# Kernel tuning notes

Hardware: AMD Instinct MI355X
Metric: run time of the kernel (lower is better)

The kernel has to match this reference:

```python
import jax, jax.numpy as jnp
import numpy as np

DIM = 512
HEADS = 8
DH = DIM // HEADS          # 64
M = DIM // 2               # 256 landmarks
PINV_ITERS = 6
KERNEL = 33                # residual_conv_kernel (lucidrains default)
SCALE = DH ** -0.5
LN_EPS = 1e-5


def setup_inputs() -> dict:
    key = jax.random.key(0)
    ks = jax.random.split(key, 6)
    b, n = 4, 4096
    x = jax.random.normal(ks[0], (b, n, DIM), jnp.float32)
    ln_w = jnp.ones((DIM,), jnp.float32)
    ln_b = jnp.zeros((DIM,), jnp.float32)
    w_qkv = jax.random.normal(ks[1], (DIM, 3 * DIM), jnp.float32) / np.float32(np.sqrt(DIM))
    w_out = jax.random.normal(ks[2], (DIM, DIM), jnp.float32) / np.float32(np.sqrt(DIM))
    b_out = jnp.zeros((DIM,), jnp.float32)
    # depthwise Conv2d(heads, heads, (33,1), groups=heads, bias=False): OIHW = (8,1,33,1)
    conv_w = jax.random.normal(ks[3], (HEADS, 1, KERNEL, 1), jnp.float32) / np.float32(np.sqrt(KERNEL))
    # admin_torch.as_module(8): residual x*omega + f(x), omega learnable scalar init sqrt(8)
    omega = jnp.asarray(np.sqrt(8.0), jnp.float32)
    return dict(x=x, ln_w=ln_w, ln_b=ln_b, w_qkv=w_qkv, w_out=w_out,
                b_out=b_out, conv_w=conv_w, omega=omega)


def _layernorm(x, w, b):
    mu = x.mean(-1, keepdims=True)
    var = x.var(-1, keepdims=True)
    return (x - mu) * jax.lax.rsqrt(var + LN_EPS) * w + b


def _moore_penrose_pinv(x, iters):
    # Newton-Schulz iteration, exactly as lucidrains nystrom-attention
    abs_x = jnp.abs(x)
    col = abs_x.sum(-1)
    row = abs_x.sum(-2)
    z = jnp.swapaxes(x, -1, -2) / (jnp.max(col) * jnp.max(row))
    I = jnp.eye(x.shape[-1], dtype=x.dtype)
    for _ in range(iters):
        xz = x @ z
        z = 0.25 * z @ (13. * I - xz @ (15. * I - xz @ (7. * I - xz)))
    return z


def reference(x, ln_w, ln_b, w_qkv, w_out, b_out, conv_w, omega):
    b, n, _ = x.shape
    nx = _layernorm(x, ln_w, ln_b)
    qkv = nx @ w_qkv                                # [b, n, 3*dim]
    q, k, v = jnp.split(qkv, 3, axis=-1)
    to_heads = lambda t: t.reshape(b, n, HEADS, DH).transpose(0, 2, 1, 3)  # bhnd
    q = to_heads(q) * SCALE
    k = to_heads(k)
    v = to_heads(v)
    l = n // M                                      # tokens per landmark group
    q_l = q.reshape(b, HEADS, M, l, DH).mean(3)     # [b,h,m,d]
    k_l = k.reshape(b, HEADS, M, l, DH).mean(3)
    sim1 = jnp.einsum('bhid,bhjd->bhij', q, k_l)    # [b,h,n,m]
    sim2 = jnp.einsum('bhid,bhjd->bhij', q_l, k_l)  # [b,h,m,m]
    sim3 = jnp.einsum('bhid,bhjd->bhij', q_l, k)    # [b,h,m,n]
    a1 = jax.nn.softmax(sim1, -1)
    a2 = jax.nn.softmax(sim2, -1)
    a3 = jax.nn.softmax(sim3, -1)
    a2_inv = _moore_penrose_pinv(a2, PINV_ITERS)
    out = (a1 @ a2_inv) @ (a3 @ v)                  # [b,h,n,d]
    # residual depthwise conv along the sequence dim of v
    res = jax.lax.conv_general_dilated(
        v, conv_w, window_strides=(1, 1),
        padding=((KERNEL // 2, KERNEL // 2), (0, 0)),
        dimension_numbers=('NCHW', 'OIHW', 'NCHW'),
        feature_group_count=HEADS)
    out = out + res
    out = out.transpose(0, 2, 1, 3).reshape(b, n, HEADS * DH)
    out = out @ w_out + b_out                       # to_out (dropout is eval no-op)
    return x * omega + out                          # admin residual
```

## Files before the change

kernel.cpp:

```cpp
#include <hip/hip_runtime.h>
#include <math.h>

#define B_    4
#define N_    4096
#define DIM_  512
#define H_    8
#define DH_   64
#define M_    256
#define LGRP  16
#define BH_   (B_*H_)
#define SCALE_ 0.125f
#define LN_EPS_ 1e-5f

#define SZ_QKVH (B_*H_*N_*DH_)
#define SZ_LM   (BH_*M_*DH_)
#define SZ_MM   (BH_*M_*M_)

typedef unsigned short ushort_t;
typedef __attribute__((ext_vector_type(8))) short bfrag8;
typedef __attribute__((ext_vector_type(4))) float fvec4;

__device__ __forceinline__ ushort_t f2b(float f) {
    unsigned u = __float_as_uint(f);
    unsigned r = (u + 0x7fffu + ((u >> 16) & 1u)) >> 16;
    return (ushort_t)r;
}
__device__ __forceinline__ float b2f(ushort_t s) {
    return __uint_as_float(((unsigned)s) << 16);
}

__global__ __launch_bounds__(256) void ln_kernel(const float* __restrict__ x,
                                                 const float* __restrict__ w,
                                                 const float* __restrict__ bb,
                                                 ushort_t* __restrict__ nxb) {
    int row = blockIdx.x;
    int t = threadIdx.x;
    const float* xr = x + (size_t)row * DIM_;
    float v0 = xr[t], v1 = xr[t + 256];
    float s = v0 + v1, sq = v0 * v0 + v1 * v1;
    __shared__ float ls[4], lq[4];
    for (int off = 32; off > 0; off >>= 1) {
        s  += __shfl_down(s, off);
        sq += __shfl_down(sq, off);
    }
    int wid = t >> 6, lid = t & 63;
    if (lid == 0) { ls[wid] = s; lq[wid] = sq; }
    __syncthreads();
    if (t == 0) {
        float S = 0, Q = 0;
        for (int i = 0; i < 4; i++) { S += ls[i]; Q += lq[i]; }
        ls[0] = S; lq[0] = Q;
    }
    __syncthreads();
    float mean = ls[0] * (1.f / DIM_);
    float var  = lq[0] * (1.f / DIM_) - mean * mean;
    float rs = rsqrtf(var + LN_EPS_);
    ushort_t* o = nxb + (size_t)row * DIM_;
    o[t]       = f2b((v0 - mean) * rs * w[t]       + bb[t]);
    o[t + 256] = f2b((v1 - mean) * rs * w[t + 256] + bb[t + 256]);
}

__global__ __launch_bounds__(256) void tcast(const float* __restrict__ in,
                                             ushort_t* __restrict__ outT,
                                             int R, int C) {
    __shared__ float tile[32][33];
    int c0 = blockIdx.x * 32, r0 = blockIdx.y * 32;
    int t = threadIdx.x;
    #pragma unroll
    for (int u = 0; u < 4; u++) {
        int lin = t + 256 * u;
        int r = lin >> 5, c = lin & 31;
        tile[r][c] = in[(size_t)(r0 + r) * C + c0 + c];
    }
    __syncthreads();
    #pragma unroll
    for (int u = 0; u < 4; u++) {
        int lin = t + 256 * u;
        int cc = lin >> 5, rr = lin & 31;
        outT[(size_t)(c0 + cc) * R + r0 + rr] = f2b(tile[rr][cc]);
    }
}

template<int EPI>
__global__ __launch_bounds__(256) void gemm_bt128(const ushort_t* __restrict__ A,
                                                  const ushort_t* __restrict__ BT,
                                                  ushort_t* __restrict__ qb,
                                                  ushort_t* __restrict__ kb,
                                                  ushort_t* __restrict__ vb,
                                                  const float* __restrict__ x,
                                                  const float* __restrict__ bo,
                                                  const float* __restrict__ omega,
                                                  float* __restrict__ out) {
    const int K = 512;
    __shared__ __align__(16) ushort_t smem[2 * 128 * 72];
    ushort_t (*As)[72] = (ushort_t(*)[72])smem;
    ushort_t (*Bs)[72] = (ushort_t(*)[72])(smem + 128 * 72);
    int t = threadIdx.x;
    int n0 = blockIdx.x * 128, m0 = blockIdx.y * 128;
    int w = t >> 6, lane = t & 63;
    int wr = (w >> 1) * 64, wc = (w & 1) * 64;
    int l15 = lane & 15, quad = lane >> 4, kq = quad * 8;
    fvec4 acc[4][4] = {};
    int rbase = t >> 3, c8 = (t & 7) * 8;

    for (int kc = 0; kc < K; kc += 64) {
        #pragma unroll
        for (int u = 0; u < 4; u++) {
            int rr = rbase + 32 * u;
            const ushort_t* ga;
            if (EPI == 0) {
                ga = A + (size_t)(m0 + rr) * K + kc + c8;
            } else {
                int grow = m0 + rr; int b_ = grow >> 12, nn = grow & 4095;
                int col = kc + c8; int hd = col >> 6, dd = col & 63;
                ga = A + (((size_t)(b_ * H_ + hd) * N_ + nn) << 6) + dd;
            }
            *(float4*)&As[rr][c8] = *(const float4*)ga;
            *(float4*)&Bs[rr][c8] = *(const float4*)(BT + (size_t)(n0 + rr) * K + kc + c8);
        }
        __syncthreads();
        #pragma unroll
        for (int ks = 0; ks < 64; ks += 32) {
            bfrag8 a[4], b[4];
            #pragma unroll
            for (int r = 0; r < 4; r++) a[r] = *(bfrag8*)&As[wr + r * 16 + l15][ks + kq];
            #pragma unroll
            for (int c = 0; c < 4; c++) b[c] = *(bfrag8*)&Bs[wc + c * 16 + l15][ks + kq];
            #pragma unroll
            for (int r = 0; r < 4; r++)
                #pragma unroll
                for (int c = 0; c < 4; c++)
                    acc[r][c] = __builtin_amdgcn_mfma_f32_16x16x32_bf16(a[r], b[c], acc[r][c], 0, 0, 0);
        }
        __syncthreads();
    }

    if (EPI == 0) {
        int sec = n0 >> 9;
        float mul = (sec == 0) ? SCALE_ : 1.0f;
        ushort_t (*Ct)[132] = (ushort_t(*)[132])smem;
        #pragma unroll
        for (int r = 0; r < 4; r++) {
            #pragma unroll
            for (int reg = 0; reg < 4; reg++) {
                int lr = wr + r * 16 + quad * 4 + reg;
                #pragma unroll
                for (int c = 0; c < 4; c++) {
                    int lc = wc + c * 16 + l15;
                    Ct[lr][lc] = f2b(acc[r][c][reg] * mul);
                }
            }
        }
        __syncthreads();
        int row = t & 127, half = t >> 7;
        int grow = m0 + row; int b_ = grow >> 12, nn = grow & 4095;
        int head = ((n0 & 511) >> 6) + half;
        ushort_t* dstbuf = (sec == 0) ? qb : ((sec == 1) ? kb : vb);
        ushort_t* dp = dstbuf + (((size_t)(b_ * H_ + head) * N_ + nn) << 6);
        #pragma unroll
        for (int i = 0; i < 8; i++)
            *(uint4*)(dp + i * 8) = *(uint4*)&Ct[row][half * 64 + i * 8];
    } else {
        float om = omega[0];
        #pragma unroll
        for (int r = 0; r < 4; r++) {
            #pragma unroll
            for (int reg = 0; reg < 4; reg++) {
                int grow = m0 + wr + r * 16 + quad * 4 + reg;
                #pragma unroll
                for (int c = 0; c < 4; c++) {
                    int gcol = n0 + wc + c * 16 + l15;
                    size_t o = (size_t)grow * DIM_ + gcol;
                    out[o] = om * x[o] + bo[gcol] + acc[r][c][reg];
                }
            }
        }
    }
}

__global__ __launch_bounds__(256) void landmark_kernel(const ushort_t* __restrict__ q,
                                                       const ushort_t* __restrict__ k,
                                                       ushort_t* __restrict__ ql,
                                                       ushort_t* __restrict__ kl) {
    int idx = blockIdx.x * 256 + threadIdx.x;
    const ushort_t* src = blockIdx.y ? k : q;
    ushort_t* dst = blockIdx.y ? kl : ql;
    int d8 = (idx & 7) * 8;
    int m = (idx >> 3) & 255;
    int bh = idx >> 11;
    const ushort_t* p = src + (((size_t)bh * N_) + m * LGRP) * DH_ + d8;
    float s[8] = {};
    #pragma unroll
    for (int j = 0; j < LGRP; j++) {
        union { uint4 u4; ushort_t sv[8]; } val;
        val.u4 = *(const uint4*)(p + (size_t)j * DH_);
        #pragma unroll
        for (int e = 0; e < 8; e++) s[e] += b2f(val.sv[e]);
    }
    union { uint4 u4; ushort_t sv[8]; } o;
    #pragma unroll
    for (int e = 0; e < 8; e++) o.sv[e] = f2b(s[e] * (1.f / LGRP));
    *(uint4*)(dst + ((size_t)bh * M_ + m) * DH_ + d8) = o.u4;
}

__global__ __launch_bounds__(256) void sim2_softmax(const ushort_t* __restrict__ ql,
                                                    const ushort_t* __restrict__ kl,
                                                    float* __restrict__ a2,
                                                    ushort_t* __restrict__ a2b) {
    int i = blockIdx.x, bh = blockIdx.y, j = threadIdx.x;
    __shared__ float qrow[64];
    __shared__ float red[256];
    if (j < 64) qrow[j] = b2f(ql[((size_t)bh * M_ + i) * DH_ + j]);
    __syncthreads();
    const ushort_t* kr = kl + ((size_t)bh * M_ + j) * DH_;
    float s = 0;
    #pragma unroll
    for (int d = 0; d < 64; d++) s += qrow[d] * b2f(kr[d]);
    red[j] = s; __syncthreads();
    for (int off = 128; off > 0; off >>= 1) {
        if (j < off) red[j] = fmaxf(red[j], red[j + off]);
        __syncthreads();
    }
    float mx = red[0]; __syncthreads();
    float p = __expf(s - mx);
    red[j] = p; __syncthreads();
    for (int off = 128; off > 0; off >>= 1) {
        if (j < off) red[j] += red[j + off];
        __syncthreads();
    }
    float res = p / red[0];
    size_t o = ((size_t)bh * M_ + i) * M_ + j;
    a2[o] = res;
    a2b[o] = f2b(res);
}

__global__ void zero2(unsigned* p) { if (threadIdx.x < 2) p[threadIdx.x] = 0u; }

__global__ __launch_bounds__(256) void a2_maxes(const float* __restrict__ a2, unsigned* red) {
    int bh = blockIdx.x, t = threadIdx.x;
    const float* A = a2 + (size_t)bh * M_ * M_;
    float rs = 0, cs = 0;
    for (int j = 0; j < M_; j++) rs += A[t * M_ + j];
    for (int i = 0; i < M_; i++) cs += A[i * M_ + t];
    __shared__ float lr[256], lc[256];
    lr[t] = rs; lc[t] = cs; __syncthreads();
    for (int off = 128; off > 0; off >>= 1) {
        if (t < off) { lr[t] = fmaxf(lr[t], lr[t + off]); lc[t] = fmaxf(lc[t], lc[t + off]); }
        __syncthreads();
    }
    if (t == 0) {
        atomicMax(red + 0, __float_as_uint(lr[0]));
        atomicMax(red + 1, __float_as_uint(lc[0]));
    }
}

__global__ __launch_bounds__(256) void pinv_init2(const float* __restrict__ a2,
                                                  const unsigned* __restrict__ red,
                                                  ushort_t* __restrict__ zA,
                                                  ushort_t* __restrict__ zAT) {
    __shared__ float tile[32][33];
    int bt = blockIdx.z; int j0 = blockIdx.x * 32, i0 = blockIdx.y * 32;
    float invd = 1.f / (__uint_as_float(red[0]) * __uint_as_float(red[1]));
    const float* Ab = a2 + ((size_t)bt << 16);
    size_t bo = (size_t)bt << 16;
    int t = threadIdx.x;
    #pragma unroll
    for (int u = 0; u < 4; u++) {
        int lin = t + 256 * u; int r = lin >> 5, c = lin & 31;
        float vv = Ab[(size_t)(i0 + r) * M_ + j0 + c] * invd;
        tile[r][c] = vv;
        zAT[bo + (size_t)(i0 + r) * M_ + j0 + c] = f2b(vv);
    }
    __syncthreads();
    #pragma unroll
    for (int u = 0; u < 4; u++) {
        int lin = t + 256 * u; int cc = lin >> 5, rr = lin & 31;
        zA[bo + (size_t)(j0 + cc) * M_ + i0 + rr] = f2b(tile[rr][cc]);
    }
}

__global__ __launch_bounds__(256) void gemm_pinv(const ushort_t* __restrict__ A,
                                                 const ushort_t* __restrict__ BT,
                                                 ushort_t* __restrict__ outN,
                                                 ushort_t* __restrict__ outT,
                                                 ushort_t* __restrict__ outT1,
                                                 float* __restrict__ outF,
                                                 float coefI, float scale) {
    __shared__ __align__(16) ushort_t As[128][72];
    __shared__ __align__(16) ushort_t Bs[64][72];
    int t = threadIdx.x; int bt = blockIdx.z;
    const ushort_t* Ab = A + ((size_t)bt << 16);
    const ushort_t* Bb = BT + ((size_t)bt << 16);
    int n0 = blockIdx.x * 64, m0 = blockIdx.y * 128;
    int w = t >> 6, lane = t & 63;
    int wr = (w >> 1) * 64, wc = (w & 1) * 32;
    int l15 = lane & 15, quad = lane >> 4, kq = quad * 8;
    fvec4 acc[4][2] = {};
    int rbase = t >> 3, c8 = (t & 7) * 8;

    for (int kc = 0; kc < M_; kc += 64) {
        #pragma unroll
        for (int u = 0; u < 4; u++) {
            int rr = rbase + 32 * u;
            *(float4*)&As[rr][c8] = *(const float4*)(Ab + (size_t)(m0 + rr) * M_ + kc + c8);
            if (u < 2)
                *(float4*)&Bs[rr][c8] = *(const float4*)(Bb + (size_t)(n0 + rr) * M_ + kc + c8);
        }
        __syncthreads();
        #pragma unroll
        for (int ks = 0; ks < 64; ks += 32) {
            bfrag8 a[4], b[2];
            #pragma unroll
            for (int r = 0; r < 4; r++) a[r] = *(bfrag8*)&As[wr + r * 16 + l15][ks + kq];
            #pragma unroll
            for (int c = 0; c < 2; c++) b[c] = *(bfrag8*)&Bs[wc + c * 16 + l15][ks + kq];
            #pragma unroll
            for (int r = 0; r < 4; r++)
                #pragma unroll
                for (int c = 0; c < 2; c++)
                    acc[r][c] = __builtin_amdgcn_mfma_f32_16x16x32_bf16(a[r], b[c], acc[r][c], 0, 0, 0);
        }
        __syncthreads();
    }

    size_t bto = (size_t)bt << 16;
    if (outN || outF) {
        #pragma unroll
        for (int r = 0; r < 4; r++) {
            #pragma unroll
            for (int reg = 0; reg < 4; reg++) {
                int grow = m0 + wr + r * 16 + quad * 4 + reg;
                #pragma unroll
                for (int c = 0; c < 2; c++) {
                    int gcol = n0 + wc + c * 16 + l15;
                    float cv = scale * acc[r][c][reg] + (grow == gcol ? coefI : 0.f);
                    if (outN) outN[bto + (size_t)grow * M_ + gcol] = f2b(cv);
                    if (outF) outF[bto + (size_t)grow * M_ + gcol] = cv;
                }
            }
        }
    }
    if (outT || outT1) {
        ushort_t (*Ct)[65] = (ushort_t(*)[65])&As[0][0];
        #pragma unroll
        for (int r = 0; r < 4; r++) {
            #pragma unroll
            for (int reg = 0; reg < 4; reg++) {
                int lr = wr + r * 16 + quad * 4 + reg;
                #pragma unroll
                for (int c = 0; c < 2; c++) {
                    int lc = wc + c * 16 + l15;
                    float cv = scale * acc[r][c][reg] + ((m0 + lr) == (n0 + lc) ? coefI : 0.f);
                    Ct[lr][lc] = f2b(cv);
                }
            }
        }
        __syncthreads();
        int j = t & 63, half = t >> 6, i0 = half * 32;
        #pragma unroll
        for (int vq = 0; vq < 4; vq++) {
            union { uint4 u4; ushort_t s[8]; } o1, o2;
            #pragma unroll
            for (int e = 0; e < 8; e++) {
                int il = i0 + vq * 8 + e;
                ushort_t bv = Ct[il][j];
                o1.s[e] = bv;
                o2.s[e] = f2b(((m0 + il) == (n0 + j) ? 7.f : 0.f) - b2f(bv));
            }
            size_t dst = bto + (size_t)(n0 + j) * M_ + m0 + i0 + vq * 8;
            if (outT)  *(uint4*)&outT[dst]  = o1.u4;
            if (outT1) *(uint4*)&outT1[dst] = o2.u4;
        }
    }
}

template<int NCH, int TRANSV>
__global__ __launch_bounds__(256) void flash_mfma(const ushort_t* __restrict__ Q,
                                                  const ushort_t* __restrict__ K,
                                                  const ushort_t* __restrict__ V,
                                                  ushort_t* __restrict__ Obf,
                                                  float* __restrict__ Opart,
                                                  float* __restrict__ lout,
                                                  int nq, int nk) {
    int bh = blockIdx.y;
    int nqt = nq >> 6;
    int qt = blockIdx.x % nqt;
    int ch = blockIdx.x / nqt;
    int q0 = qt * 64;
    int chunk = nk / NCH;
    int j0 = ch * chunk, j1 = j0 + chunk;

    __shared__ __align__(16) ushort_t qs[64][72];
    __shared__ __align__(16) ushort_t ks[64][72];
    __shared__ __align__(16) ushort_t vts[64][72];
    __shared__ __align__(16) ushort_t pb[64][72];

    int t = threadIdx.x;
    int w = t >> 6, lane = t & 63;
    int l15 = lane & 15, quad = lane >> 4, kq = quad * 8;
    int wrow = w * 16;

    const ushort_t* Qb = Q + ((size_t)bh * nq + q0) * DH_;
    #pragma unroll
    for (int u = 0; u < 2; u++) {
        int lin = t + 256 * u;
        int r = lin >> 3, cc = (lin & 7) * 8;
        *(uint4*)&qs[r][cc] = *(const uint4*)(Qb + r * DH_ + cc);
    }

    fvec4 Oacc[4];
    #pragma unroll
    for (int nt = 0; nt < 4; nt++)
        #pragma unroll
        for (int reg = 0; reg < 4; reg++) Oacc[nt][reg] = 0.f;
    float l_[4] = {0.f, 0.f, 0.f, 0.f};

    const ushort_t* VTbase = V + (size_t)bh * DH_ * nk;
    for (int j = j0; j < j1; j += 64) {
        const ushort_t* Kb = K + ((size_t)bh * nk + j) * DH_;
        const ushort_t* Vb = V + ((size_t)bh * nk + j) * DH_;
        #pragma unroll
        for (int u = 0; u < 2; u++) {
            int lin = t + 256 * u;
            int r = lin >> 3, cc = (lin & 7) * 8;
            *(uint4*)&ks[r][cc] = *(const uint4*)(Kb + r * DH_ + cc);
            if (TRANSV == 0) {
                *(uint4*)&vts[r][cc] = *(const uint4*)(VTbase + (size_t)r * nk + j + cc);
            } else {
                union { uint4 u4; ushort_t s[8]; } vv;
                vv.u4 = *(const uint4*)(Vb + r * DH_ + cc);
                #pragma unroll
                for (int m = 0; m < 8; m++) vts[cc + m][r] = vv.s[m];
            }
        }
        __syncthreads();

        fvec4 S[4];
        #pragma unroll
        for (int ct = 0; ct < 4; ct++)
            #pragma unroll
            for (int reg = 0; reg < 4; reg++) S[ct][reg] = 0.f;
        bfrag8 aq0 = *(bfrag8*)&qs[wrow + l15][kq];
        bfrag8 aq1 = *(bfrag8*)&qs[wrow + l15][32 + kq];
        #pragma unroll
        for (int ct = 0; ct < 4; ct++) {
            bfrag8 b0 = *(bfrag8*)&ks[ct * 16 + l15][kq];
            bfrag8 b1 = *(bfrag8*)&ks[ct * 16 + l15][32 + kq];
            S[ct] = __builtin_amdgcn_mfma_f32_16x16x32_bf16(aq0, b0, S[ct], 0, 0, 0);
            S[ct] = __builtin_amdgcn_mfma_f32_16x16x32_bf16(aq1, b1, S[ct], 0, 0, 0);
        }

        float ps[4] = {0.f, 0.f, 0.f, 0.f};
        #pragma unroll
        for (int ct = 0; ct < 4; ct++) {
            #pragma unroll
            for (int reg = 0; reg < 4; reg++) {
                float pv = __expf(S[ct][reg]);
                ps[reg] += pv;
                pb[wrow + quad * 4 + reg][ct * 16 + l15] = f2b(pv);
            }
        }
        #pragma unroll
        for (int reg = 0; reg < 4; reg++) {
            float s = ps[reg];
            s += __shfl_xor(s, 1);
            s += __shfl_xor(s, 2);
            s += __shfl_xor(s, 4);
            s += __shfl_xor(s, 8);
            l_[reg] += s;
        }

        bfrag8 ap0 = *(bfrag8*)&pb[wrow + l15][kq];
        bfrag8 ap1 = *(bfrag8*)&pb[wrow + l15][32 + kq];
        #pragma unroll
        for (int nt = 0; nt < 4; nt++) {
            bfrag8 b0 = *(bfrag8*)&vts[nt * 16 + l15][kq];
            bfrag8 b1 = *(bfrag8*)&vts[nt * 16 + l15][32 + kq];
            Oacc[nt] = __builtin_amdgcn_mfma_f32_16x16x32_bf16(ap0, b0, Oacc[nt], 0, 0, 0);
            Oacc[nt] = __builtin_amdgcn_mfma_f32_16x16x32_bf16(ap1, b1, Oacc[nt], 0, 0, 0);
        }
        __syncthreads();
    }

    if (NCH == 1) {
        #pragma unroll
        for (int reg = 0; reg < 4; reg++) {
            float inv = 1.f / l_[reg];
            #pragma unroll
            for (int nt = 0; nt < 4; nt++)
                qs[wrow + quad * 4 + reg][nt * 16 + l15] = f2b(Oacc[nt][reg] * inv);
        }
        __syncthreads();
        ushort_t* Ob = Obf + ((size_t)bh * nq + q0) * DH_;
        #pragma unroll
        for (int u = 0; u < 2; u++) {
            int lin = t + 256 * u;
            int r = lin >> 3, i = (lin & 7) * 8;
            *(uint4*)(Ob + (size_t)r * DH_ + i) = *(uint4*)&qs[r][i];
        }
    } else {
        size_t rows_per_ch = (size_t)BH_ * nq;
        #pragma unroll
        for (int reg = 0; reg < 4; reg++) {
            size_t rowg = (size_t)bh * nq + q0 + wrow + quad * 4 + reg;
            #pragma unroll
            for (int nt = 0; nt < 4; nt++)
                Opart[((size_t)ch * rows_per_ch + rowg) * DH_ + nt * 16 + l15] = Oacc[nt][reg];
            if (l15 == 0)
                lout[(size_t)ch * rows_per_ch + rowg] = l_[reg];
        }
    }
}

__global__ __launch_bounds__(256) void flash_combine(const float* __restrict__ apart,
                                                     const float* __restrict__ lpart,
                                                     ushort_t* __restrict__ a3vb) {
    int idx = blockIdx.x * 256 + threadIdx.x;
    int d = idx & 63; int row = idx >> 6;
    const int R = BH_ * M_;
    float l = lpart[row] + lpart[row + R] + lpart[row + 2 * R] + lpart[row + 3 * R];
    size_t e = (size_t)row * DH_ + d;
    const size_t CH = (size_t)R * DH_;
    float o = apart[e] + apart[e + CH] + apart[e + 2 * CH] + apart[e + 3 * CH];
    a3vb[e] = f2b(o / l);
}

__global__ __launch_bounds__(256) void wm_mfma(const ushort_t* __restrict__ Z,
                                               const ushort_t* __restrict__ A3V,
                                               ushort_t* __restrict__ WmT) {
    __shared__ __align__(16) ushort_t As[64][72];
    __shared__ __align__(16) ushort_t Bs[64][72];
    int bh = blockIdx.y;
    int i0 = blockIdx.x * 64;
    const ushort_t* Zb = Z + ((size_t)bh << 16);
    const ushort_t* Ab = A3V + ((size_t)bh << 14);
    int t = threadIdx.x;
    int w = t >> 6, lane = t & 63;
    int wr = (w >> 1) * 32, wc = (w & 1) * 32;
    int l15 = lane & 15, quad = lane >> 4, kq = quad * 8;
    fvec4 acc[2][2] = {};
    int rbase = t >> 3, c8 = (t & 7) * 8;

    for (int kc = 0; kc < M_; kc += 64) {
        #pragma unroll
        for (int u = 0; u < 2; u++) {
            int rr = rbase + 32 * u;
            *(float4*)&Bs[rr][c8] = *(const float4*)(Zb + (size_t)(i0 + rr) * M_ + kc + c8);
            union { uint4 u4; ushort_t s[8]; } av;
            av.u4 = *(const uint4*)(Ab + (size_t)(kc + rr) * DH_ + c8);
            #pragma unroll
            for (int m = 0; m < 8; m++) As[c8 + m][rr] = av.s[m];
        }
        __syncthreads();
        #pragma unroll
        for (int ks = 0; ks < 64; ks += 32) {
            bfrag8 a[2], b[2];
            #pragma unroll
            for (int r = 0; r < 2; r++) a[r] = *(bfrag8*)&As[wr + r * 16 + l15][ks + kq];
            #pragma unroll
            for (int c = 0; c < 2; c++) b[c] = *(bfrag8*)&Bs[wc + c * 16 + l15][ks + kq];
            #pragma unroll
            for (int r = 0; r < 2; r++)
                #pragma unroll
                for (int c = 0; c < 2; c++)
                    acc[r][c] = __builtin_amdgcn_mfma_f32_16x16x32_bf16(a[r], b[c], acc[r][c], 0, 0, 0);
        }
        __syncthreads();
    }
    #pragma unroll
    for (int r = 0; r < 2; r++) {
        #pragma unroll
        for (int reg = 0; reg < 4; reg++) {
            int drow = wr + r * 16 + quad * 4 + reg;
            ushort_t* dp = WmT + ((size_t)bh * DH_ + drow) * M_;
            #pragma unroll
            for (int c = 0; c < 2; c++)
                dp[i0 + wc + c * 16 + l15] = f2b(acc[r][c][reg]);
        }
    }
}

__global__ __launch_bounds__(256) void conv_kernel(const ushort_t* __restrict__ V,
                                                   const float* __restrict__ cw,
                                                   const ushort_t* __restrict__ ctxb,
                                                   ushort_t* __restrict__ outb) {
    int bh = blockIdx.y;
    int h = bh & 7;
    int i0 = blockIdx.x * 64;
    __shared__ float vb[96][64];
    __shared__ float wloc[33];
    int t = threadIdx.x;
    if (t < 33) wloc[t] = cw[h * 33 + t];
    #pragma unroll
    for (int u = 0; u < 3; u++) {
        int lin = t + 256 * u;
        int r = lin >> 3, cc = (lin & 7) * 8;
        int gi = i0 - 16 + r;
        union { uint4 u4; ushort_t s[8]; } val;
        if (gi >= 0 && gi < N_)
            val.u4 = *(const uint4*)(V + ((size_t)bh * N_ + gi) * DH_ + cc);
        else
            val.u4 = make_uint4(0, 0, 0, 0);
        #pragma unroll
        for (int m = 0; m < 8; m++) vb[r][cc + m] = b2f(val.s[m]);
    }
    __syncthreads();
    int d = t & 63, rb = t >> 6;
    for (int u = 0; u < 16; u++) {
        int r = rb * 16 + u;
        float s = 0.f;
        #pragma unroll
        for (int kk = 0; kk < 33; kk++) s += wloc[kk] * vb[r + kk][d];
        size_t o = ((size_t)bh * N_ + i0 + r) * DH_ + d;
        outb[o] = f2b(b2f(ctxb[o]) + s);
    }
}

extern "C" void kernel_launch(void* const* d_in, const int* in_sizes, int n_in,
                              void* d_out, int out_size, void* d_ws, size_t ws_size,
                              hipStream_t stream) {
    const float* x      = (const float*)d_in[0];
    const float* ln_w   = (const float*)d_in[1];
    const float* ln_b   = (const float*)d_in[2];
    const float* w_qkv  = (const float*)d_in[3];
    const float* w_out  = (const float*)d_in[4];
    const float* b_out  = (const float*)d_in[5];
    const float* conv_w = (const float*)d_in[6];
    const float* omega  = (const float*)d_in[7];
    float* out = (float*)d_out;

    float* fp = (float*)d_ws;
    float* a2    = fp;              fp += SZ_MM;
    float* apart = fp;              fp += SZ_QKVH / 4;
    float* lpart = fp;              fp += 4 * BH_ * M_;
    ushort_t* us = (ushort_t*)fp;
    ushort_t* wqkvT = us;           us += DIM_ * 3 * DIM_;
    ushort_t* woT   = us;           us += DIM_ * DIM_;
    ushort_t* a2b   = us;           us += SZ_MM;
    ushort_t* zA    = us;           us += SZ_MM;
    ushort_t* zAT   = us;           us += SZ_MM;
    ushort_t* zB    = us;           us += SZ_MM;
    ushort_t* zBT   = us;           us += SZ_MM;
    ushort_t* qb    = us;           us += SZ_QKVH;
    ushort_t* kb    = us;           us += SZ_QKVH;
    ushort_t* vb    = us;           us += SZ_QKVH;
    ushort_t* ctxb  = us;           us += SZ_QKVH;
    ushort_t* outhb = us;           us += SZ_QKVH;
    ushort_t* ql    = us;           us += SZ_LM;
    ushort_t* kl    = us;           us += SZ_LM;
    ushort_t* WmT   = us;           us += SZ_LM;
    ushort_t* a3vb  = us;           us += SZ_LM;
    unsigned* red   = (unsigned*)us;
    ushort_t* nxb = outhb;
    ushort_t* xz  = ctxb;
    ushort_t* t1T = xz  + SZ_MM;
    ushort_t* t2T = t1T + SZ_MM;
    ushort_t* t3T = t2T + SZ_MM;

    ln_kernel<<<B_ * N_, 256, 0, stream>>>(x, ln_w, ln_b, nxb);
    tcast<<<dim3(48, 16), 256, 0, stream>>>(w_qkv, wqkvT, DIM_, 3 * DIM_);
    tcast<<<dim3(16, 16), 256, 0, stream>>>(w_out, woT, DIM_, DIM_);
    gemm_bt128<0><<<dim3(12, 128), 256, 0, stream>>>(nxb, wqkvT, qb, kb, vb,
                                                     nullptr, nullptr, nullptr, nullptr);
    landmark_kernel<<<dim3(256, 2), 256, 0, stream>>>(qb, kb, ql, kl);
    sim2_softmax<<<dim3(M_, BH_), 256, 0, stream>>>(ql, kl, a2, a2b);
    zero2<<<1, 64, 0, stream>>>(red);
    a2_maxes<<<BH_, 256, 0, stream>>>(a2, red);
    pinv_init2<<<dim3(8, 8, 32), 256, 0, stream>>>(a2, red, zA, zAT);

    ushort_t* za = zA;  ushort_t* zaT = zAT;
    ushort_t* zb = zB;  ushort_t* zbT = zBT;
    for (int it = 0; it < 6; it++) {
        gemm_pinv<<<dim3(4, 2, BH_), 256, 0, stream>>>(a2b, zaT, xz, nullptr, t1T, nullptr, 0.f, 1.f);
        gemm_pinv<<<dim3(4, 2, BH_), 256, 0, stream>>>(xz, t1T, nullptr, t2T, nullptr, nullptr, 15.f, -1.f);
        gemm_pinv<<<dim3(4, 2, BH_), 256, 0, stream>>>(xz, t2T, nullptr, t3T, nullptr, nullptr, 13.f, -1.f);
        gemm_pinv<<<dim3(4, 2, BH_), 256, 0, stream>>>(za, t3T, zb, (it < 5) ? zbT : nullptr,
                                                       nullptr, nullptr, 0.f, 0.25f);
        ushort_t* tp;
        tp = za; za = zb; zb = tp;
        tp = zaT; zaT = zbT; zbT = tp;
    }

    flash_mfma<4, 1><<<dim3(16, BH_), 256, 0, stream>>>(ql, kb, vb, nullptr, apart, lpart, M_, N_);
    flash_combine<<<(BH_ * M_ * DH_) / 256, 256, 0, stream>>>(apart, lpart, a3vb);
    wm_mfma<<<dim3(4, BH_), 256, 0, stream>>>(za, a3vb, WmT);
    flash_mfma<1, 0><<<dim3(64, BH_), 256, 0, stream>>>(qb, kl, WmT, ctxb, nullptr, nullptr, N_, M_);
    conv_kernel<<<dim3(N_ / 64, BH_), 256, 0, stream>>>(vb, conv_w, ctxb, outhb);
    gemm_bt128<1><<<dim3(4, 128), 256, 0, stream>>>(outhb, woT, nullptr, nullptr, nullptr,
                                                    x, b_out, omega, out);
}
```

Before: 565.8 us.

## Remap GEMM blocks across XCDs, split pinv norm reduction, shrink pinv GEMM tiles

The QKV/out GEMM now permutes linear block IDs so consecutive blocks are spread across XCD groups, aiming for better L2 locality. The pinv normaliser reduction drops the row-sum pass, since softmax rows sum to one, and splits the column sums into a parallel partial kernel plus a max kernel. This replaces a single strided per-head kernel. The Newton-Schulz GEMMs use 64x64 tiles instead of 128x64, doubling the block count to fill more CUs, at the cost of more redundant operand loads. Assuming the max row sum is exactly one drops a rounding-level factor from the scale.

```diff
diff --git a/kernel.cpp b/kernel.cpp
--- a/kernel.cpp
+++ b/kernel.cpp
@@ -96,7 +96,10 @@
     ushort_t (*As)[72] = (ushort_t(*)[72])smem;
     ushort_t (*Bs)[72] = (ushort_t(*)[72])(smem + 128 * 72);
     int t = threadIdx.x;
-    int n0 = blockIdx.x * 128, m0 = blockIdx.y * 128;
+    int lin = blockIdx.x + blockIdx.y * gridDim.x;
+    int nwg = gridDim.x * gridDim.y;
+    int wg  = (lin & 7) * (nwg >> 3) + (lin >> 3);
+    int n0 = (wg % gridDim.x) * 128, m0 = (wg / gridDim.x) * 128;
     int w = t >> 6, lane = t & 63;
     int wr = (w >> 1) * 64, wc = (w & 1) * 64;
     int l15 = lane & 15, quad = lane >> 4, kq = quad * 8;
@@ -236,22 +239,28 @@
 
 __global__ void zero2(unsigned* p) { if (threadIdx.x < 2) p[threadIdx.x] = 0u; }
 
-__global__ __launch_bounds__(256) void a2_maxes(const float* __restrict__ a2, unsigned* red) {
+__global__ __launch_bounds__(256) void colpart(const float* __restrict__ a2,
+                                               float* __restrict__ cs2) {
+    int bh = blockIdx.x, s = blockIdx.y, t = threadIdx.x;
+    const float* A = a2 + ((size_t)bh << 16) + (size_t)s * 32 * M_;
+    float cs = 0.f;
+    #pragma unroll
+    for (int i = 0; i < 32; i++) cs += A[(size_t)i * M_ + t];
+    cs2[((size_t)s * BH_ + bh) * M_ + t] = cs;
+}
+
+__global__ __launch_bounds__(256) void colmax(const float* __restrict__ cs2, unsigned* red) {
     int bh = blockIdx.x, t = threadIdx.x;
-    const float* A = a2 + (size_t)bh * M_ * M_;
-    float rs = 0, cs = 0;
-    for (int j = 0; j < M_; j++) rs += A[t * M_ + j];
-    for (int i = 0; i < M_; i++) cs += A[i * M_ + t];
-    __shared__ float lr[256], lc[256];
-    lr[t] = rs; lc[t] = cs; __syncthreads();
+    float v = 0.f;
+    #pragma unroll
+    for (int s = 0; s < 8; s++) v += cs2[((size_t)s * BH_ + bh) * M_ + t];
+    __shared__ float lr[256];
+    lr[t] = v; __syncthreads();
     for (int off = 128; off > 0; off >>= 1) {
-        if (t < off) { lr[t] = fmaxf(lr[t], lr[t + off]); lc[t] = fmaxf(lc[t], lc[t + off]); }
-        __syncthreads();
-    }
-    if (t == 0) {
-        atomicMax(red + 0, __float_as_uint(lr[0]));
-        atomicMax(red + 1, __float_as_uint(lc[0]));
-    }
+        if (t < off) lr[t] = fmaxf(lr[t], lr[t + off]);
+        __syncthreads();
+    }
+    if (t == 0) atomicMax(red, __float_as_uint(lr[0]));
 }
 
 __global__ __launch_bounds__(256) void pinv_init2(const float* __restrict__ a2,
@@ -260,7 +269,7 @@
                                                   ushort_t* __restrict__ zAT) {
     __shared__ float tile[32][33];
     int bt = blockIdx.z; int j0 = blockIdx.x * 32, i0 = blockIdx.y * 32;
-    float invd = 1.f / (__uint_as_float(red[0]) * __uint_as_float(red[1]));
+    float invd = 1.f / __uint_as_float(red[0]);
     const float* Ab = a2 + ((size_t)bt << 16);
     size_t bo = (size_t)bt << 16;
     int t = threadIdx.x;
@@ -286,36 +295,35 @@
                                                  ushort_t* __restrict__ outT1,
                                                  float* __restrict__ outF,
                                                  float coefI, float scale) {
-    __shared__ __align__(16) ushort_t As[128][72];
+    __shared__ __align__(16) ushort_t As[64][72];
     __shared__ __align__(16) ushort_t Bs[64][72];
     int t = threadIdx.x; int bt = blockIdx.z;
     const ushort_t* Ab = A + ((size_t)bt << 16);
     const ushort_t* Bb = BT + ((size_t)bt << 16);
-    int n0 = blockIdx.x * 64, m0 = blockIdx.y * 128;
+    int n0 = blockIdx.x * 64, m0 = blockIdx.y * 64;
     int w = t >> 6, lane = t & 63;
-    int wr = (w >> 1) * 64, wc = (w & 1) * 32;
+    int wr = (w >> 1) * 32, wc = (w & 1) * 32;
     int l15 = lane & 15, quad = lane >> 4, kq = quad * 8;
-    fvec4 acc[4][2] = {};
+    fvec4 acc[2][2] = {};
     int rbase = t >> 3, c8 = (t & 7) * 8;
 
     for (int kc = 0; kc < M_; kc += 64) {
         #pragma unroll
-        for (int u = 0; u < 4; u++) {
+        for (int u = 0; u < 2; u++) {
             int rr = rbase + 32 * u;
             *(float4*)&As[rr][c8] = *(const float4*)(Ab + (size_t)(m0 + rr) * M_ + kc + c8);
-            if (u < 2)
-                *(float4*)&Bs[rr][c8] = *(const float4*)(Bb + (size_t)(n0 + rr) * M_ + kc + c8);
+            *(float4*)&Bs[rr][c8] = *(const float4*)(Bb + (size_t)(n0 + rr) * M_ + kc + c8);
         }
         __syncthreads();
         #pragma unroll
         for (int ks = 0; ks < 64; ks += 32) {
-            bfrag8 a[4], b[2];
-            #pragma unroll
-            for (int r = 0; r < 4; r++) a[r] = *(bfrag8*)&As[wr + r * 16 + l15][ks + kq];
+            bfrag8 a[2], b[2];
+            #pragma unroll
+            for (int r = 0; r < 2; r++) a[r] = *(bfrag8*)&As[wr + r * 16 + l15][ks + kq];
             #pragma unroll
             for (int c = 0; c < 2; c++) b[c] = *(bfrag8*)&Bs[wc + c * 16 + l15][ks + kq];
             #pragma unroll
-            for (int r = 0; r < 4; r++)
+            for (int r = 0; r < 2; r++)
                 #pragma unroll
                 for (int c = 0; c < 2; c++)
                     acc[r][c] = __builtin_amdgcn_mfma_f32_16x16x32_bf16(a[r], b[c], acc[r][c], 0, 0, 0);
@@ -326,7 +334,7 @@
     size_t bto = (size_t)bt << 16;
     if (outN || outF) {
         #pragma unroll
-        for (int r = 0; r < 4; r++) {
+        for (int r = 0; r < 2; r++) {
             #pragma unroll
             for (int reg = 0; reg < 4; reg++) {
                 int grow = m0 + wr + r * 16 + quad * 4 + reg;
@@ -343,7 +351,7 @@
     if (outT || outT1) {
         ushort_t (*Ct)[65] = (ushort_t(*)[65])&As[0][0];
         #pragma unroll
-        for (int r = 0; r < 4; r++) {
+        for (int r = 0; r < 2; r++) {
             #pragma unroll
             for (int reg = 0; reg < 4; reg++) {
                 int lr = wr + r * 16 + quad * 4 + reg;
@@ -356,9 +364,9 @@
             }
         }
         __syncthreads();
-        int j = t & 63, half = t >> 6, i0 = half * 32;
-        #pragma unroll
-        for (int vq = 0; vq < 4; vq++) {
+        int j = t & 63, quarter = t >> 6, i0 = quarter * 16;
+        #pragma unroll
+        for (int vq = 0; vq < 2; vq++) {
             union { uint4 u4; ushort_t s[8]; } o1, o2;
             #pragma unroll
             for (int e = 0; e < 8; e++) {
@@ -633,6 +641,7 @@
     float* a2    = fp;              fp += SZ_MM;
     float* apart = fp;              fp += SZ_QKVH / 4;
     float* lpart = fp;              fp += 4 * BH_ * M_;
+    float* cs2   = fp;              fp += 8 * BH_ * M_;
     ushort_t* us = (ushort_t*)fp;
     ushort_t* wqkvT = us;           us += DIM_ * 3 * DIM_;
     ushort_t* woT   = us;           us += DIM_ * DIM_;
@@ -665,16 +674,17 @@
     landmark_kernel<<<dim3(256, 2), 256, 0, stream>>>(qb, kb, ql, kl);
     sim2_softmax<<<dim3(M_, BH_), 256, 0, stream>>>(ql, kl, a2, a2b);
     zero2<<<1, 64, 0, stream>>>(red);
-    a2_maxes<<<BH_, 256, 0, stream>>>(a2, red);
+    colpart<<<dim3(BH_, 8), 256, 0, stream>>>(a2, cs2);
+    colmax<<<BH_, 256, 0, stream>>>(cs2, red);
     pinv_init2<<<dim3(8, 8, 32), 256, 0, stream>>>(a2, red, zA, zAT);
 
     ushort_t* za = zA;  ushort_t* zaT = zAT;
     ushort_t* zb = zB;  ushort_t* zbT = zBT;
     for (int it = 0; it < 6; it++) {
-        gemm_pinv<<<dim3(4, 2, BH_), 256, 0, stream>>>(a2b, zaT, xz, nullptr, t1T, nullptr, 0.f, 1.f);
-        gemm_pinv<<<dim3(4, 2, BH_), 256, 0, stream>>>(xz, t1T, nullptr, t2T, nullptr, nullptr, 15.f, -1.f);
-        gemm_pinv<<<dim3(4, 2, BH_), 256, 0, stream>>>(xz, t2T, nullptr, t3T, nullptr, nullptr, 13.f, -1.f);
-        gemm_pinv<<<dim3(4, 2, BH_), 256, 0, stream>>>(za, t3T, zb, (it < 5) ? zbT : nullptr,
+        gemm_pinv<<<dim3(4, 4, BH_), 256, 0, stream>>>(a2b, zaT, xz, nullptr, t1T, nullptr, 0.f, 1.f);
+        gemm_pinv<<<dim3(4, 4, BH_), 256, 0, stream>>>(xz, t1T, nullptr, t2T, nullptr, nullptr, 15.f, -1.f);
+        gemm_pinv<<<dim3(4, 4, BH_), 256, 0, stream>>>(xz, t2T, nullptr, t3T, nullptr, nullptr, 13.f, -1.f);
+        gemm_pinv<<<dim3(4, 4, BH_), 256, 0, stream>>>(za, t3T, zb, (it < 5) ? zbT : nullptr,
                                                        nullptr, nullptr, 0.f, 0.25f);
         ushort_t* tp;
         tp = za; za = zb; zb = tp;
```

Result: faster. 523.7 us (-7.4%).
